# Kernel optimization log

Measured on AMD Instinct MI355X. Metric: run time of the kernel, lower is better.

The kernel has to match this reference:

```python
import jax, jax.numpy as jnp
import numpy as np

B, T, D, H = 2, 2048, 1024, 16
DH = D // H

def setup_inputs() -> dict:
    key = jax.random.key(0)
    ks = jax.random.split(key, 6)
    s = 0.02
    return {
        "x": jax.random.normal(ks[0], (B, T, D), jnp.float32),
        "Wq": jax.random.normal(ks[1], (D, D), jnp.float32) * s,
        "Wk": jax.random.normal(ks[2], (D, D), jnp.float32) * s,
        "Wv": jax.random.normal(ks[3], (D, D), jnp.float32) * s,
        "Wo": jax.random.normal(ks[4], (D, D), jnp.float32) * s,
        "bo": jnp.zeros((D,), jnp.float32),
    }

def reference(x, Wq, Wk, Wv, Wo, bo):
    Bx, Tx, _ = x.shape
    # project and split heads: [B, H, T, DH]
    q = (x @ Wq).reshape(Bx, Tx, H, DH).transpose(0, 2, 1, 3)
    k = (x @ Wk).reshape(Bx, Tx, H, DH).transpose(0, 2, 1, 3)
    v = (x @ Wv).reshape(Bx, Tx, H, DH).transpose(0, 2, 1, 3)
    scores = jnp.einsum("bhqd,bhkd->bhqk", q, k)  # [B,H,T,T]
    causal = jnp.triu(jnp.ones((Tx, Tx), bool), k=1)  # True above diagonal
    scores = jnp.where(causal, -jnp.inf, scores)
    # original scales AFTER masking (equivalent math)
    w = jax.nn.softmax(scores / jnp.sqrt(jnp.float32(DH)), axis=-1)
    # dropout p=0.0 -> identity
    ctx = jnp.einsum("bhqk,bhkd->bhqd", w, v)
    ctx = ctx.transpose(0, 2, 1, 3).reshape(Bx, Tx, D)
    return ctx @ Wo + bo
```

## Files before the change

kernel.cpp:

```cpp
#include <hip/hip_runtime.h>
#include <hip/hip_bf16.h>


typedef __bf16 bf16x8 __attribute__((ext_vector_type(8)));
typedef __bf16 bf16x4 __attribute__((ext_vector_type(4)));
typedef float  f32x4  __attribute__((ext_vector_type(4)));

#define Bx 2
#define Tx 2048
#define Dx 1024
#define Hx 16
#define DHx 64

__global__ __launch_bounds__(256) void prep(const float* __restrict__ x,
                                            const float* __restrict__ W0,
                                            const float* __restrict__ W1,
                                            const float* __restrict__ W2,
                                            const float* __restrict__ W3,
                                            __bf16* __restrict__ xb,
                                            __bf16* __restrict__ Wt) {
    const int z = blockIdx.z;
    if (z == 0) {
        const int blk = blockIdx.y * 16 + blockIdx.x;
        const float* xp = x + (size_t)blk * 16384;
        __bf16* xo = xb + (size_t)blk * 16384;
#pragma unroll
        for (int i = 0; i < 16; i++) {
            float4 v = *(const float4*)(xp + i * 1024 + threadIdx.x * 4);
            bf16x4 o;
            o[0] = (__bf16)v.x; o[1] = (__bf16)v.y; o[2] = (__bf16)v.z; o[3] = (__bf16)v.w;
            *(bf16x4*)(xo + i * 1024 + threadIdx.x * 4) = o;
        }
        return;
    }
    __shared__ float tile[64][65];
    const float* W = (z == 1) ? W0 : (z == 2) ? W1 : (z == 3) ? W2 : W3;
    __bf16* o = Wt + (size_t)(z - 1) * Dx * Dx;
    int k0 = blockIdx.x * 64, n0 = blockIdx.y * 64;
    int t = threadIdx.x;
    int cc = t & 63, rbase = t >> 6;
#pragma unroll
    for (int i = 0; i < 16; i++) {
        int rr = rbase + i * 4;
        tile[rr][cc] = W[(size_t)(k0 + rr) * Dx + n0 + cc];
    }
    __syncthreads();
#pragma unroll
    for (int i = 0; i < 16; i++) {
        int rr = rbase + i * 4;
        o[(size_t)(n0 + rr) * Dx + k0 + cc] = (__bf16)tile[cc][rr];
    }
}

static __device__ __forceinline__ void gload16(const __bf16* g, __bf16* l) {
    __builtin_amdgcn_global_load_lds((const __attribute__((address_space(1))) void*)g,
                                     (__attribute__((address_space(3))) void*)l, 16, 0, 0);
}

__global__ __launch_bounds__(256, 3) void gemm_qkv(const __bf16* __restrict__ A,
                                                   const __bf16* __restrict__ BT,
                                                   __bf16* __restrict__ Qb,
                                                   __bf16* __restrict__ Kb,
                                                   __bf16* __restrict__ Vt) {
    __shared__ __bf16 As[2][128 * 32];
    __shared__ __bf16 Bs[2][128 * 32];
    const int t = threadIdx.x;
    const int lane = t & 63, wave = t >> 6;
    const int lane15 = lane & 15, quad = lane >> 4;
    const int m0 = blockIdx.x * 128, n0 = blockIdx.y * 128;
    const int wm = wave & 1, wn = wave >> 1;

    const int sr = wave * 16 + (lane >> 2);
    const int sc = (lane & 3) * 8;
    const __bf16* Ag = A + (size_t)(m0 + sr) * Dx + sc;
    const __bf16* Bg = BT + (size_t)(n0 + sr) * Dx + sc;
    __bf16* As00 = &As[0][(wave * 16) * 32];
    __bf16* As01 = &As[0][(64 + wave * 16) * 32];
    __bf16* As10 = &As[1][(wave * 16) * 32];
    __bf16* As11 = &As[1][(64 + wave * 16) * 32];
    __bf16* Bs00 = &Bs[0][(wave * 16) * 32];
    __bf16* Bs01 = &Bs[0][(64 + wave * 16) * 32];
    __bf16* Bs10 = &Bs[1][(wave * 16) * 32];
    __bf16* Bs11 = &Bs[1][(64 + wave * 16) * 32];

    f32x4 acc[4][4];
#pragma unroll
    for (int i = 0; i < 4; i++)
#pragma unroll
        for (int j = 0; j < 4; j++) acc[i][j] = (f32x4){0.f, 0.f, 0.f, 0.f};

    for (int k0 = 0; k0 < Dx; k0 += 64) {
        gload16(Ag, As00);
        gload16(Ag + 64 * Dx, As01);
        gload16(Ag + 32, As10);
        gload16(Ag + 64 * Dx + 32, As11);
        gload16(Bg, Bs00);
        gload16(Bg + 64 * Dx, Bs01);
        gload16(Bg + 32, Bs10);
        gload16(Bg + 64 * Dx + 32, Bs11);
        Ag += 64; Bg += 64;
        __syncthreads();
#pragma unroll
        for (int half = 0; half < 2; half++) {
            bf16x8 af[4], bfr[4];
#pragma unroll
            for (int i = 0; i < 4; i++)
                af[i] = *(const bf16x8*)&As[half][(wm * 64 + i * 16 + lane15) * 32 + quad * 8];
#pragma unroll
            for (int j = 0; j < 4; j++)
                bfr[j] = *(const bf16x8*)&Bs[half][(wn * 64 + j * 16 + lane15) * 32 + quad * 8];
#pragma unroll
            for (int mt = 0; mt < 4; mt++)
#pragma unroll
                for (int nt = 0; nt < 4; nt++)
                    acc[mt][nt] = __builtin_amdgcn_mfma_f32_16x16x32_bf16(af[mt], bfr[nt], acc[mt][nt], 0, 0, 0);
        }
        __syncthreads();
    }

    const int z = n0 >> 10;
    if (z < 2) {
        __bf16* outp = z ? Kb : Qb;
        const float scale = z ? 1.0f : 0.18033688011112042f;
#pragma unroll
        for (int mt = 0; mt < 4; mt++)
#pragma unroll
            for (int nt = 0; nt < 4; nt++) {
                const int cc = (n0 + wn * 64 + nt * 16 + lane15) & 1023;
                const int h = cc >> 6, dh = cc & 63;
#pragma unroll
                for (int r4 = 0; r4 < 4; r4++) {
                    const int row = m0 + wm * 64 + mt * 16 + quad * 4 + r4;
                    const int b = row >> 11, tt = row & 2047;
                    outp[(((size_t)(b * Hx + h) * Tx + tt) << 6) + dh] =
                        (__bf16)(acc[mt][nt][r4] * scale);
                }
            }
    } else {
#pragma unroll
        for (int mt = 0; mt < 4; mt++)
#pragma unroll
            for (int nt = 0; nt < 4; nt++) {
                const int cc = (n0 + wn * 64 + nt * 16 + lane15) & 1023;
                const int h = cc >> 6, dh = cc & 63;
#pragma unroll
                for (int r4 = 0; r4 < 4; r4++) {
                    const int row = m0 + wm * 64 + mt * 16 + quad * 4 + r4;
                    const int b = row >> 11, tt = row & 2047;
                    Vt[((size_t)(b * Hx + h) * DHx + dh) * Tx + tt] = (__bf16)acc[mt][nt][r4];
                }
            }
    }
}

__global__ __launch_bounds__(256, 2) void gemm_out(const __bf16* __restrict__ A,
                                                   const __bf16* __restrict__ BT,
                                                   float* __restrict__ outf,
                                                   const float* __restrict__ bias) {
    __shared__ __bf16 As[2][128 * 32];
    __shared__ __bf16 Bs[2][64 * 32];
    const int t = threadIdx.x;
    const int lane = t & 63, wave = t >> 6;
    const int lane15 = lane & 15, quad = lane >> 4;
    const int m0 = blockIdx.x * 128, n0 = blockIdx.y * 64;
    const int wm = wave & 1, wn = wave >> 1;

    const int sr = wave * 16 + (lane >> 2), sc = (lane & 3) * 8;
    const __bf16* Ag = A + (size_t)(m0 + sr) * Dx + sc;
    const __bf16* Bg = BT + (size_t)(n0 + sr) * Dx + sc;
    __bf16* As00 = &As[0][(wave * 16) * 32];
    __bf16* As01 = &As[0][(64 + wave * 16) * 32];
    __bf16* As10 = &As[1][(wave * 16) * 32];
    __bf16* As11 = &As[1][(64 + wave * 16) * 32];
    __bf16* Bs0  = &Bs[0][(wave * 16) * 32];
    __bf16* Bs1  = &Bs[1][(wave * 16) * 32];

    f32x4 acc[4][2];
#pragma unroll
    for (int i = 0; i < 4; i++)
#pragma unroll
        for (int j = 0; j < 2; j++) acc[i][j] = (f32x4){0.f, 0.f, 0.f, 0.f};

    for (int k0 = 0; k0 < Dx; k0 += 64) {
        gload16(Ag, As00);
        gload16(Ag + 64 * Dx, As01);
        gload16(Ag + 32, As10);
        gload16(Ag + 64 * Dx + 32, As11);
        gload16(Bg, Bs0);
        gload16(Bg + 32, Bs1);
        Ag += 64; Bg += 64;
        __syncthreads();
#pragma unroll
        for (int half = 0; half < 2; half++) {
            bf16x8 af[4], bfr[2];
#pragma unroll
            for (int i = 0; i < 4; i++)
                af[i] = *(const bf16x8*)&As[half][(wm * 64 + i * 16 + lane15) * 32 + quad * 8];
#pragma unroll
            for (int j = 0; j < 2; j++)
                bfr[j] = *(const bf16x8*)&Bs[half][(wn * 32 + j * 16 + lane15) * 32 + quad * 8];
#pragma unroll
            for (int mt = 0; mt < 4; mt++)
#pragma unroll
                for (int nt = 0; nt < 2; nt++)
                    acc[mt][nt] = __builtin_amdgcn_mfma_f32_16x16x32_bf16(af[mt], bfr[nt], acc[mt][nt], 0, 0, 0);
        }
        __syncthreads();
    }

#pragma unroll
    for (int mt = 0; mt < 4; mt++)
#pragma unroll
        for (int nt = 0; nt < 2; nt++) {
            const int col = n0 + wn * 32 + nt * 16 + lane15;
#pragma unroll
            for (int r4 = 0; r4 < 4; r4++) {
                const int row = m0 + wm * 64 + mt * 16 + quad * 4 + r4;
                outf[(size_t)row * Dx + col] = acc[mt][nt][r4] + bias[col];
            }
        }
}

__global__ __launch_bounds__(256) void attn_mfma(const __bf16* __restrict__ Q,
                                                 const __bf16* __restrict__ K,
                                                 const __bf16* __restrict__ Vt,
                                                 __bf16* __restrict__ ctx) {
    __shared__ __bf16 Ks[64 * 72];
    __shared__ __bf16 Vs[64 * 72];
    __shared__ __bf16 Ps[64 * 72];
    const int t = threadIdx.x;
    const int lane = t & 63, wave = t >> 6;
    const int lane15 = lane & 15, quad = lane >> 4;
    const int id = blockIdx.x;
    const int bh = id & 31, p = id >> 5;
    const int b = bh >> 4, h = bh & 15;
    const size_t headoff = ((size_t)(b * Hx + h)) * Tx * DHx;
    const __bf16* Kbase = K + headoff;
    const __bf16* Vbase = Vt + headoff;
    const int sr = t >> 2, sc = (t & 3) * 16;

    for (int cidx = 0; cidx < 2; cidx++) {
        const int chunk = (cidx == 0) ? (31 - p) : p;
        const int ktiles = chunk + 1;
        const int q0 = chunk * 64;
        const int qg = q0 + wave * 16 + quad * 4;

        bf16x8 qf0, qf1;
        {
            const __bf16* Qp = Q + headoff + (size_t)(q0 + wave * 16 + lane15) * 64 + quad * 8;
            qf0 = *(const bf16x8*)Qp;
            qf1 = *(const bf16x8*)(Qp + 32);
        }
        f32x4 o[4];
#pragma unroll
        for (int i = 0; i < 4; i++) o[i] = (f32x4){0.f, 0.f, 0.f, 0.f};
        float lpart[4] = {0.f, 0.f, 0.f, 0.f};

        bf16x8 kpre0, kpre1, vpre0, vpre1;
        {
            const __bf16* Kp = Kbase + (size_t)sr * 64 + sc;
            kpre0 = *(const bf16x8*)Kp; kpre1 = *(const bf16x8*)(Kp + 8);
            const __bf16* Vp = Vbase + (size_t)sr * Tx + sc;
            vpre0 = *(const bf16x8*)Vp; vpre1 = *(const bf16x8*)(Vp + 8);
        }

        for (int kt = 0; kt < ktiles; kt++) {
            __syncthreads();
            *(bf16x8*)&Ks[sr * 72 + sc] = kpre0;
            *(bf16x8*)&Ks[sr * 72 + sc + 8] = kpre1;
            *(bf16x8*)&Vs[sr * 72 + sc] = vpre0;
            *(bf16x8*)&Vs[sr * 72 + sc + 8] = vpre1;
            if (kt + 1 < ktiles) {
                const __bf16* Kp = Kbase + (size_t)((kt + 1) * 64 + sr) * 64 + sc;
                kpre0 = *(const bf16x8*)Kp; kpre1 = *(const bf16x8*)(Kp + 8);
                const __bf16* Vp = Vbase + (size_t)sr * Tx + (kt + 1) * 64 + sc;
                vpre0 = *(const bf16x8*)Vp; vpre1 = *(const bf16x8*)(Vp + 8);
            } else if (cidx == 0) {
                const __bf16* Kp = Kbase + (size_t)sr * 64 + sc;
                kpre0 = *(const bf16x8*)Kp; kpre1 = *(const bf16x8*)(Kp + 8);
                const __bf16* Vp = Vbase + (size_t)sr * Tx + sc;
                vpre0 = *(const bf16x8*)Vp; vpre1 = *(const bf16x8*)(Vp + 8);
            }
            __syncthreads();

            f32x4 s[4];
            __builtin_amdgcn_s_setprio(1);
#pragma unroll
            for (int nt = 0; nt < 4; nt++) {
                s[nt] = (f32x4){0.f, 0.f, 0.f, 0.f};
                bf16x8 b0 = *(const bf16x8*)&Ks[(nt * 16 + lane15) * 72 + quad * 8];
                s[nt] = __builtin_amdgcn_mfma_f32_16x16x32_bf16(qf0, b0, s[nt], 0, 0, 0);
                bf16x8 b1 = *(const bf16x8*)&Ks[(nt * 16 + lane15) * 72 + 32 + quad * 8];
                s[nt] = __builtin_amdgcn_mfma_f32_16x16x32_bf16(qf1, b1, s[nt], 0, 0, 0);
            }
            __builtin_amdgcn_s_setprio(0);

            if (kt == ktiles - 1) {
                const int kbase = kt * 64;
#pragma unroll
                for (int nt = 0; nt < 4; nt++)
#pragma unroll
                    for (int reg = 0; reg < 4; reg++) {
                        float e = __builtin_amdgcn_exp2f(s[nt][reg]);
                        if (kbase + nt * 16 + lane15 > qg + reg) e = 0.f;
                        lpart[reg] += e;
                        Ps[(wave * 16 + quad * 4 + reg) * 72 + nt * 16 + lane15] = (__bf16)e;
                    }
            } else {
#pragma unroll
                for (int nt = 0; nt < 4; nt++)
#pragma unroll
                    for (int reg = 0; reg < 4; reg++) {
                        float e = __builtin_amdgcn_exp2f(s[nt][reg]);
                        lpart[reg] += e;
                        Ps[(wave * 16 + quad * 4 + reg) * 72 + nt * 16 + lane15] = (__bf16)e;
                    }
            }

            bf16x8 pa0 = *(const bf16x8*)&Ps[(wave * 16 + lane15) * 72 + quad * 8];
            bf16x8 pa1 = *(const bf16x8*)&Ps[(wave * 16 + lane15) * 72 + 32 + quad * 8];
            __builtin_amdgcn_s_setprio(1);
#pragma unroll
            for (int dt = 0; dt < 4; dt++) {
                bf16x8 vb0 = *(const bf16x8*)&Vs[(dt * 16 + lane15) * 72 + quad * 8];
                o[dt] = __builtin_amdgcn_mfma_f32_16x16x32_bf16(pa0, vb0, o[dt], 0, 0, 0);
                bf16x8 vb1 = *(const bf16x8*)&Vs[(dt * 16 + lane15) * 72 + 32 + quad * 8];
                o[dt] = __builtin_amdgcn_mfma_f32_16x16x32_bf16(pa1, vb1, o[dt], 0, 0, 0);
            }
            __builtin_amdgcn_s_setprio(0);
        }

        float inv[4];
#pragma unroll
        for (int reg = 0; reg < 4; reg++) {
            float l = lpart[reg];
#pragma unroll
            for (int off = 1; off < 16; off <<= 1) l += __shfl_xor(l, off);
            inv[reg] = 1.f / l;
        }
#pragma unroll
        for (int dt = 0; dt < 4; dt++)
#pragma unroll
            for (int reg = 0; reg < 4; reg++) {
                int q = q0 + wave * 16 + quad * 4 + reg;
                ctx[(((size_t)(b * Tx + q)) * Hx + h) * 64 + dt * 16 + lane15] =
                    (__bf16)(o[dt][reg] * inv[reg]);
            }
    }
}

extern "C" void kernel_launch(void* const* d_in, const int* in_sizes, int n_in,
                              void* d_out, int out_size, void* d_ws, size_t ws_size,
                              hipStream_t stream) {
    const float* x  = (const float*)d_in[0];
    const float* Wq = (const float*)d_in[1];
    const float* Wk = (const float*)d_in[2];
    const float* Wv = (const float*)d_in[3];
    const float* Wo = (const float*)d_in[4];
    const float* bo = (const float*)d_in[5];
    float* out = (float*)d_out;

    char* ws = (char*)d_ws;
    __bf16* xb  = (__bf16*)(ws + 0);
    __bf16* Wt  = (__bf16*)(ws + (8ull << 20));
    __bf16* Qb  = (__bf16*)(ws + (16ull << 20));
    __bf16* Kb  = (__bf16*)(ws + (24ull << 20));
    __bf16* Vtg = (__bf16*)(ws + (32ull << 20));
    __bf16* ctx = (__bf16*)(ws + (40ull << 20));

    prep<<<dim3(16, 16, 5), 256, 0, stream>>>(x, Wq, Wk, Wv, Wo, xb, Wt);

    gemm_qkv<<<dim3(Bx * Tx / 128, 3 * Dx / 128), 256, 0, stream>>>(xb, Wt, Qb, Kb, Vtg);

    attn_mfma<<<dim3(512), 256, 0, stream>>>(Qb, Kb, Vtg, ctx);

    gemm_out<<<dim3(Bx * Tx / 128, Dx / 64), 256, 0, stream>>>(ctx, Wt + 3 * (1u << 20), out, bo);
}
```

Measured before the change: 171.3 us.

## Split long causal attention chunks across two blocks with partial-sum merge kernel

Replaces the paired-chunk attention schedule (each block handling chunk 31-p then p) with a table of 47 work items per head. Query chunks 17-31 have their KV range split in two, and the two partial outputs and row sums go to fp32 workspace. A new norm kernel adds the two partials and divides by the summed denominators to produce ctx for rows 1088 and up. This raises the block count from 512 to 1504 and evens out per-block work. In exchange it adds an extra launch, fp32 partial traffic, and recomputed Q loads.

```diff
diff --git a/kernel.cpp b/kernel.cpp
--- a/kernel.cpp
+++ b/kernel.cpp
@@ -11,6 +11,20 @@
 #define Dx 1024
 #define Hx 16
 #define DHx 64
+
+__device__ __constant__ unsigned char JTAB[47][3] = {
+    {16, 0, 17},
+    {31, 0, 16}, {31, 16, 16}, {30, 0, 16}, {15, 0, 16},
+    {30, 16, 15}, {29, 0, 15}, {29, 15, 15}, {28, 0, 15}, {14, 0, 15},
+    {28, 15, 14}, {27, 0, 14}, {27, 14, 14}, {26, 0, 14}, {13, 0, 14},
+    {26, 14, 13}, {25, 0, 13}, {25, 13, 13}, {24, 0, 13}, {12, 0, 13},
+    {24, 13, 12}, {23, 0, 12}, {23, 12, 12}, {22, 0, 12}, {11, 0, 12},
+    {22, 12, 11}, {21, 0, 11}, {21, 11, 11}, {20, 0, 11}, {10, 0, 11},
+    {20, 11, 10}, {19, 0, 10}, {19, 10, 10}, {18, 0, 10}, {9, 0, 10},
+    {18, 10, 9}, {17, 0, 9}, {17, 9, 9}, {8, 0, 9},
+    {7, 0, 8}, {6, 0, 7}, {5, 0, 6}, {4, 0, 5}, {3, 0, 4}, {2, 0, 3},
+    {1, 0, 2}, {0, 0, 1}
+};
 
 __global__ __launch_bounds__(256) void prep(const float* __restrict__ x,
                                             const float* __restrict__ W0,
@@ -224,7 +238,10 @@
 __global__ __launch_bounds__(256) void attn_mfma(const __bf16* __restrict__ Q,
                                                  const __bf16* __restrict__ K,
                                                  const __bf16* __restrict__ Vt,
-                                                 __bf16* __restrict__ ctx) {
+                                                 __bf16* __restrict__ ctx,
+                                                 float* __restrict__ o0w,
+                                                 float* __restrict__ o1w,
+                                                 float* __restrict__ lw) {
     __shared__ __bf16 Ks[64 * 72];
     __shared__ __bf16 Vs[64 * 72];
     __shared__ __bf16 Ps[64 * 72];
@@ -232,121 +249,155 @@
     const int lane = t & 63, wave = t >> 6;
     const int lane15 = lane & 15, quad = lane >> 4;
     const int id = blockIdx.x;
-    const int bh = id & 31, p = id >> 5;
+    const int j = id >> 5, bh = id & 31;
+    const int c = JTAB[j][0];
+    const int t0 = JTAB[j][1];
+    const int ktend = t0 + JTAB[j][2];
+    const bool single = (t0 == 0) && (ktend == c + 1);
     const int b = bh >> 4, h = bh & 15;
+    const int q0 = c * 64;
+    const int qg = q0 + wave * 16 + quad * 4;
     const size_t headoff = ((size_t)(b * Hx + h)) * Tx * DHx;
     const __bf16* Kbase = K + headoff;
     const __bf16* Vbase = Vt + headoff;
     const int sr = t >> 2, sc = (t & 3) * 16;
 
-    for (int cidx = 0; cidx < 2; cidx++) {
-        const int chunk = (cidx == 0) ? (31 - p) : p;
-        const int ktiles = chunk + 1;
-        const int q0 = chunk * 64;
-        const int qg = q0 + wave * 16 + quad * 4;
-
-        bf16x8 qf0, qf1;
-        {
-            const __bf16* Qp = Q + headoff + (size_t)(q0 + wave * 16 + lane15) * 64 + quad * 8;
-            qf0 = *(const bf16x8*)Qp;
-            qf1 = *(const bf16x8*)(Qp + 32);
-        }
-        f32x4 o[4];
-#pragma unroll
-        for (int i = 0; i < 4; i++) o[i] = (f32x4){0.f, 0.f, 0.f, 0.f};
-        float lpart[4] = {0.f, 0.f, 0.f, 0.f};
-
-        bf16x8 kpre0, kpre1, vpre0, vpre1;
-        {
-            const __bf16* Kp = Kbase + (size_t)sr * 64 + sc;
+    bf16x8 qf0, qf1;
+    {
+        const __bf16* Qp = Q + headoff + (size_t)(q0 + wave * 16 + lane15) * 64 + quad * 8;
+        qf0 = *(const bf16x8*)Qp;
+        qf1 = *(const bf16x8*)(Qp + 32);
+    }
+    f32x4 o[4];
+#pragma unroll
+    for (int i = 0; i < 4; i++) o[i] = (f32x4){0.f, 0.f, 0.f, 0.f};
+    float lpart[4] = {0.f, 0.f, 0.f, 0.f};
+
+    bf16x8 kpre0, kpre1, vpre0, vpre1;
+    {
+        const __bf16* Kp = Kbase + (size_t)(t0 * 64 + sr) * 64 + sc;
+        kpre0 = *(const bf16x8*)Kp; kpre1 = *(const bf16x8*)(Kp + 8);
+        const __bf16* Vp = Vbase + (size_t)sr * Tx + t0 * 64 + sc;
+        vpre0 = *(const bf16x8*)Vp; vpre1 = *(const bf16x8*)(Vp + 8);
+    }
+
+    for (int kt = t0; kt < ktend; kt++) {
+        __syncthreads();
+        *(bf16x8*)&Ks[sr * 72 + sc] = kpre0;
+        *(bf16x8*)&Ks[sr * 72 + sc + 8] = kpre1;
+        *(bf16x8*)&Vs[sr * 72 + sc] = vpre0;
+        *(bf16x8*)&Vs[sr * 72 + sc + 8] = vpre1;
+        if (kt + 1 < ktend) {
+            const __bf16* Kp = Kbase + (size_t)((kt + 1) * 64 + sr) * 64 + sc;
             kpre0 = *(const bf16x8*)Kp; kpre1 = *(const bf16x8*)(Kp + 8);
-            const __bf16* Vp = Vbase + (size_t)sr * Tx + sc;
+            const __bf16* Vp = Vbase + (size_t)sr * Tx + (kt + 1) * 64 + sc;
             vpre0 = *(const bf16x8*)Vp; vpre1 = *(const bf16x8*)(Vp + 8);
         }
-
-        for (int kt = 0; kt < ktiles; kt++) {
-            __syncthreads();
-            *(bf16x8*)&Ks[sr * 72 + sc] = kpre0;
-            *(bf16x8*)&Ks[sr * 72 + sc + 8] = kpre1;
-            *(bf16x8*)&Vs[sr * 72 + sc] = vpre0;
-            *(bf16x8*)&Vs[sr * 72 + sc + 8] = vpre1;
-            if (kt + 1 < ktiles) {
-                const __bf16* Kp = Kbase + (size_t)((kt + 1) * 64 + sr) * 64 + sc;
-                kpre0 = *(const bf16x8*)Kp; kpre1 = *(const bf16x8*)(Kp + 8);
-                const __bf16* Vp = Vbase + (size_t)sr * Tx + (kt + 1) * 64 + sc;
-                vpre0 = *(const bf16x8*)Vp; vpre1 = *(const bf16x8*)(Vp + 8);
-            } else if (cidx == 0) {
-                const __bf16* Kp = Kbase + (size_t)sr * 64 + sc;
-                kpre0 = *(const bf16x8*)Kp; kpre1 = *(const bf16x8*)(Kp + 8);
-                const __bf16* Vp = Vbase + (size_t)sr * Tx + sc;
-                vpre0 = *(const bf16x8*)Vp; vpre1 = *(const bf16x8*)(Vp + 8);
-            }
-            __syncthreads();
-
-            f32x4 s[4];
-            __builtin_amdgcn_s_setprio(1);
-#pragma unroll
-            for (int nt = 0; nt < 4; nt++) {
-                s[nt] = (f32x4){0.f, 0.f, 0.f, 0.f};
-                bf16x8 b0 = *(const bf16x8*)&Ks[(nt * 16 + lane15) * 72 + quad * 8];
-                s[nt] = __builtin_amdgcn_mfma_f32_16x16x32_bf16(qf0, b0, s[nt], 0, 0, 0);
-                bf16x8 b1 = *(const bf16x8*)&Ks[(nt * 16 + lane15) * 72 + 32 + quad * 8];
-                s[nt] = __builtin_amdgcn_mfma_f32_16x16x32_bf16(qf1, b1, s[nt], 0, 0, 0);
-            }
-            __builtin_amdgcn_s_setprio(0);
-
-            if (kt == ktiles - 1) {
-                const int kbase = kt * 64;
-#pragma unroll
-                for (int nt = 0; nt < 4; nt++)
-#pragma unroll
-                    for (int reg = 0; reg < 4; reg++) {
-                        float e = __builtin_amdgcn_exp2f(s[nt][reg]);
-                        if (kbase + nt * 16 + lane15 > qg + reg) e = 0.f;
-                        lpart[reg] += e;
-                        Ps[(wave * 16 + quad * 4 + reg) * 72 + nt * 16 + lane15] = (__bf16)e;
-                    }
-            } else {
-#pragma unroll
-                for (int nt = 0; nt < 4; nt++)
-#pragma unroll
-                    for (int reg = 0; reg < 4; reg++) {
-                        float e = __builtin_amdgcn_exp2f(s[nt][reg]);
-                        lpart[reg] += e;
-                        Ps[(wave * 16 + quad * 4 + reg) * 72 + nt * 16 + lane15] = (__bf16)e;
-                    }
-            }
-
-            bf16x8 pa0 = *(const bf16x8*)&Ps[(wave * 16 + lane15) * 72 + quad * 8];
-            bf16x8 pa1 = *(const bf16x8*)&Ps[(wave * 16 + lane15) * 72 + 32 + quad * 8];
-            __builtin_amdgcn_s_setprio(1);
-#pragma unroll
-            for (int dt = 0; dt < 4; dt++) {
-                bf16x8 vb0 = *(const bf16x8*)&Vs[(dt * 16 + lane15) * 72 + quad * 8];
-                o[dt] = __builtin_amdgcn_mfma_f32_16x16x32_bf16(pa0, vb0, o[dt], 0, 0, 0);
-                bf16x8 vb1 = *(const bf16x8*)&Vs[(dt * 16 + lane15) * 72 + 32 + quad * 8];
-                o[dt] = __builtin_amdgcn_mfma_f32_16x16x32_bf16(pa1, vb1, o[dt], 0, 0, 0);
-            }
-            __builtin_amdgcn_s_setprio(0);
-        }
-
-        float inv[4];
-#pragma unroll
-        for (int reg = 0; reg < 4; reg++) {
-            float l = lpart[reg];
-#pragma unroll
-            for (int off = 1; off < 16; off <<= 1) l += __shfl_xor(l, off);
-            inv[reg] = 1.f / l;
-        }
+        __syncthreads();
+
+        f32x4 s[4];
+        __builtin_amdgcn_s_setprio(1);
+#pragma unroll
+        for (int nt = 0; nt < 4; nt++) {
+            s[nt] = (f32x4){0.f, 0.f, 0.f, 0.f};
+            bf16x8 b0 = *(const bf16x8*)&Ks[(nt * 16 + lane15) * 72 + quad * 8];
+            s[nt] = __builtin_amdgcn_mfma_f32_16x16x32_bf16(qf0, b0, s[nt], 0, 0, 0);
+            bf16x8 b1 = *(const bf16x8*)&Ks[(nt * 16 + lane15) * 72 + 32 + quad * 8];
+            s[nt] = __builtin_amdgcn_mfma_f32_16x16x32_bf16(qf1, b1, s[nt], 0, 0, 0);
+        }
+        __builtin_amdgcn_s_setprio(0);
+
+        if (kt == c) {
+            const int kbase = kt * 64;
+#pragma unroll
+            for (int nt = 0; nt < 4; nt++)
+#pragma unroll
+                for (int reg = 0; reg < 4; reg++) {
+                    float e = __builtin_amdgcn_exp2f(s[nt][reg]);
+                    if (kbase + nt * 16 + lane15 > qg + reg) e = 0.f;
+                    lpart[reg] += e;
+                    Ps[(wave * 16 + quad * 4 + reg) * 72 + nt * 16 + lane15] = (__bf16)e;
+                }
+        } else {
+#pragma unroll
+            for (int nt = 0; nt < 4; nt++)
+#pragma unroll
+                for (int reg = 0; reg < 4; reg++) {
+                    float e = __builtin_amdgcn_exp2f(s[nt][reg]);
+                    lpart[reg] += e;
+                    Ps[(wave * 16 + quad * 4 + reg) * 72 + nt * 16 + lane15] = (__bf16)e;
+                }
+        }
+
+        bf16x8 pa0 = *(const bf16x8*)&Ps[(wave * 16 + lane15) * 72 + quad * 8];
+        bf16x8 pa1 = *(const bf16x8*)&Ps[(wave * 16 + lane15) * 72 + 32 + quad * 8];
+        __builtin_amdgcn_s_setprio(1);
+#pragma unroll
+        for (int dt = 0; dt < 4; dt++) {
+            bf16x8 vb0 = *(const bf16x8*)&Vs[(dt * 16 + lane15) * 72 + quad * 8];
+            o[dt] = __builtin_amdgcn_mfma_f32_16x16x32_bf16(pa0, vb0, o[dt], 0, 0, 0);
+            bf16x8 vb1 = *(const bf16x8*)&Vs[(dt * 16 + lane15) * 72 + 32 + quad * 8];
+            o[dt] = __builtin_amdgcn_mfma_f32_16x16x32_bf16(pa1, vb1, o[dt], 0, 0, 0);
+        }
+        __builtin_amdgcn_s_setprio(0);
+    }
+
+    float lsum[4];
+#pragma unroll
+    for (int reg = 0; reg < 4; reg++) {
+        float l = lpart[reg];
+#pragma unroll
+        for (int off = 1; off < 16; off <<= 1) l += __shfl_xor(l, off);
+        lsum[reg] = l;
+    }
+
+    if (single) {
 #pragma unroll
         for (int dt = 0; dt < 4; dt++)
 #pragma unroll
             for (int reg = 0; reg < 4; reg++) {
                 int q = q0 + wave * 16 + quad * 4 + reg;
                 ctx[(((size_t)(b * Tx + q)) * Hx + h) * 64 + dt * 16 + lane15] =
-                    (__bf16)(o[dt][reg] * inv[reg]);
+                    (__bf16)(o[dt][reg] / lsum[reg]);
             }
-    }
+    } else {
+        float* op = (t0 == 0) ? o0w : o1w;
+        const int tr0 = q0 - 1088 + wave * 16 + quad * 4;
+#pragma unroll
+        for (int dt = 0; dt < 4; dt++)
+#pragma unroll
+            for (int reg = 0; reg < 4; reg++)
+                op[((size_t)(b * 960 + tr0 + reg) << 10) + h * 64 + dt * 16 + lane15] =
+                    o[dt][reg];
+        if (lane15 == 0) {
+            const int slot = (t0 == 0) ? 0 : 1;
+            float* lp = lw + ((size_t)(slot * Bx + b) * Hx + h) * 960 + tr0;
+#pragma unroll
+            for (int reg = 0; reg < 4; reg++) lp[reg] = lsum[reg];
+        }
+    }
+}
+
+__global__ __launch_bounds__(256) void norm(const float* __restrict__ o0w,
+                                            const float* __restrict__ o1w,
+                                            const float* __restrict__ lw,
+                                            __bf16* __restrict__ ctx) {
+    const int r = blockIdx.x;
+    const int b = r / 960, tr = r % 960;
+    const int tid = threadIdx.x;
+    const int h = tid >> 4;
+    const size_t rowoff = ((size_t)(b * 960 + tr) << 10) + tid * 4;
+    float4 a = *(const float4*)(o0w + rowoff);
+    float4 c4 = *(const float4*)(o1w + rowoff);
+    const float l0 = lw[((size_t)(0 * Bx + b) * Hx + h) * 960 + tr];
+    const float l1 = lw[((size_t)(1 * Bx + b) * Hx + h) * 960 + tr];
+    const float inv = 1.f / (l0 + l1);
+    bf16x4 o;
+    o[0] = (__bf16)((a.x + c4.x) * inv);
+    o[1] = (__bf16)((a.y + c4.y) * inv);
+    o[2] = (__bf16)((a.z + c4.z) * inv);
+    o[3] = (__bf16)((a.w + c4.w) * inv);
+    *(bf16x4*)(ctx + (((size_t)(b * Tx + 1088 + tr)) << 10) + tid * 4) = o;
 }
 
 extern "C" void kernel_launch(void* const* d_in, const int* in_sizes, int n_in,
@@ -367,12 +418,17 @@
     __bf16* Kb  = (__bf16*)(ws + (24ull << 20));
     __bf16* Vtg = (__bf16*)(ws + (32ull << 20));
     __bf16* ctx = (__bf16*)(ws + (40ull << 20));
+    float*  o0w = (float*)(ws + (48ull << 20));
+    float*  o1w = (float*)(ws + (56ull << 20));
+    float*  lw  = (float*)(ws + (64ull << 20));
 
     prep<<<dim3(16, 16, 5), 256, 0, stream>>>(x, Wq, Wk, Wv, Wo, xb, Wt);
 
     gemm_qkv<<<dim3(Bx * Tx / 128, 3 * Dx / 128), 256, 0, stream>>>(xb, Wt, Qb, Kb, Vtg);
 
-    attn_mfma<<<dim3(512), 256, 0, stream>>>(Qb, Kb, Vtg, ctx);
+    attn_mfma<<<dim3(1504), 256, 0, stream>>>(Qb, Kb, Vtg, ctx, o0w, o1w, lw);
+
+    norm<<<dim3(1920), 256, 0, stream>>>(o0w, o1w, lw, ctx);
 
     gemm_out<<<dim3(Bx * Tx / 128, Dx / 64), 256, 0, stream>>>(ctx, Wt + 3 * (1u << 20), out, bo);
 }
```

Result: no change. 173.2 us (+1.1%).
